# Kernel tuning notes

Measured on AMD Instinct MI355X. Metric: run time of the kernel, lower is better.

The kernel has to match this reference:

```python
import jax, jax.numpy as jnp
import numpy as np

B, L, D = 4, 2048, 1024
E, K, H = 8, 2, 4096
EPS = 1e-5


def setup_inputs() -> dict:
    key = jax.random.key(0)
    ks = jax.random.split(key, 6)
    x = jax.random.normal(ks[0], (B, L, D), jnp.float32)
    gate_w = jax.random.normal(ks[1], (E, D), jnp.float32) * 0.02
    W1 = jax.random.normal(ks[2], (E, D, H), jnp.float32) * 0.02
    b1 = jnp.zeros((E, H), jnp.float32)
    W2 = jax.random.normal(ks[3], (E, H, D), jnp.float32) * 0.02
    b2 = jnp.zeros((E, D), jnp.float32)
    gamma = jnp.ones((D,), jnp.float32)
    beta = jnp.zeros((D,), jnp.float32)
    return {"x": x, "gamma": gamma, "beta": beta, "gate_w": gate_w,
            "W1": W1, "b1": b1, "W2": W2, "b2": b2}


def reference(x, gamma, beta, gate_w, W1, b1, W2, b2):
    # LayerNorm (biased variance, eps=1e-5, matches torch.nn.LayerNorm)
    mu = jnp.mean(x, axis=-1, keepdims=True)
    var = jnp.mean((x - mu) ** 2, axis=-1, keepdims=True)
    xn = (x - mu) / jnp.sqrt(var + EPS) * gamma + beta
    xf = xn.reshape(-1, D)  # (T, D), T = B*L
    T = xf.shape[0]

    # gating: top-k logits -> softmax -> scatter into dense gates (T, E)
    logits = xf @ gate_w.T  # (T, E)
    top_v, top_i = jax.lax.top_k(logits, K)
    top_g = jax.nn.softmax(top_v, axis=-1)
    gates = jnp.zeros_like(logits).at[jnp.arange(T)[:, None], top_i].set(top_g)

    # experts: dense-equivalent of masked gather/FFN/scatter-add combine.
    # Non-selected experts contribute with gate weight 0 -> identical math.
    h = jax.nn.gelu(jnp.einsum('td,edh->teh', xf, W1) + b1, approximate=False)
    y = jnp.einsum('teh,ehd->ted', h, W2) + b2  # (T, E, D)
    out = jnp.einsum('te,ted->td', gates, y).reshape(B, L, D) + x

    # load-balance loss: MSE(mean gate per expert, uniform)
    load = jnp.mean(gates, axis=0)
    bal_loss = jnp.mean((load - 1.0 / E) ** 2)
    return out, bal_loss
```

## Files before the change

kernel.cpp:

```cpp
#include <hip/hip_runtime.h>
#include <hip/hip_bf16.h>

#define T_TOK 8192
#define DD 1024
#define EE 8
#define HH 4096
#define NA (2 * T_TOK)
#define NBLK (NA / 256)

typedef __bf16 bf16_t;
typedef __bf16 bf16x8 __attribute__((ext_vector_type(8)));
typedef __bf16 bf16x4 __attribute__((ext_vector_type(4)));
typedef float f32x4 __attribute__((ext_vector_type(4)));

#define GLDS(g, l) __builtin_amdgcn_global_load_lds( \
    (const __attribute__((address_space(1))) void*)(g), \
    (__attribute__((address_space(3))) void*)(l), 16, 0, 0)

__global__ __launch_bounds__(256) void ln_gate_kernel(
    const float* __restrict__ x, const float* __restrict__ gamma,
    const float* __restrict__ beta, const float* __restrict__ gate_w,
    bf16_t* __restrict__ xn, int* __restrict__ tokexp, float* __restrict__ tokgate)
{
    const int t = blockIdx.x;
    const int tid = threadIdx.x;
    const int lane = tid & 63, wave = tid >> 6;
    __shared__ float wred[4];
    __shared__ float stats[2];
    __shared__ float lred[32];
    __shared__ float logitsS[8];

    float4 v = ((const float4*)(x + (size_t)t * DD))[tid];
    float s = v.x + v.y + v.z + v.w;
#pragma unroll
    for (int o = 32; o > 0; o >>= 1) s += __shfl_down(s, o, 64);
    if (lane == 0) wred[wave] = s;
    __syncthreads();
    if (tid == 0) stats[0] = (wred[0] + wred[1] + wred[2] + wred[3]) * (1.0f / DD);
    __syncthreads();
    const float mu = stats[0];
    float d0 = v.x - mu, d1 = v.y - mu, d2 = v.z - mu, d3 = v.w - mu;
    float q = d0*d0 + d1*d1 + d2*d2 + d3*d3;
#pragma unroll
    for (int o = 32; o > 0; o >>= 1) q += __shfl_down(q, o, 64);
    __syncthreads();
    if (lane == 0) wred[wave] = q;
    __syncthreads();
    if (tid == 0) stats[1] = rsqrtf((wred[0]+wred[1]+wred[2]+wred[3]) * (1.0f / DD) + 1e-5f);
    __syncthreads();
    const float rstd = stats[1];
    float4 g4 = ((const float4*)gamma)[tid];
    float4 b4 = ((const float4*)beta)[tid];
    float n0 = d0 * rstd * g4.x + b4.x;
    float n1 = d1 * rstd * g4.y + b4.y;
    float n2 = d2 * rstd * g4.z + b4.z;
    float n3 = d3 * rstd * g4.w + b4.w;
    bf16x4 pk = { (bf16_t)n0, (bf16_t)n1, (bf16_t)n2, (bf16_t)n3 };
    ((bf16x4*)(xn + (size_t)t * DD))[tid] = pk;

    float part[8];
#pragma unroll
    for (int e = 0; e < 8; ++e) {
        float4 gw = ((const float4*)(gate_w + (size_t)e * DD))[tid];
        part[e] = n0 * gw.x + n1 * gw.y + n2 * gw.z + n3 * gw.w;
    }
#pragma unroll
    for (int e = 0; e < 8; ++e) {
        float p = part[e];
#pragma unroll
        for (int o = 32; o > 0; o >>= 1) p += __shfl_down(p, o, 64);
        if (lane == 0) lred[wave * 8 + e] = p;
    }
    __syncthreads();
    if (tid < 8) logitsS[tid] = lred[tid] + lred[8 + tid] + lred[16 + tid] + lred[24 + tid];
    __syncthreads();
    if (tid == 0) {
        float best = -1e30f; int e0 = 0;
        for (int e = 0; e < 8; ++e) { float le = logitsS[e]; if (le > best) { best = le; e0 = e; } }
        float best2 = -1e30f; int e1 = (e0 == 0) ? 1 : 0;
        for (int e = 0; e < 8; ++e) if (e != e0) { float le = logitsS[e]; if (le > best2) { best2 = le; e1 = e; } }
        float z = expf(best2 - best);
        float g0 = 1.0f / (1.0f + z);
        float g1 = z * g0;
        tokexp[2*t] = e0; tokexp[2*t+1] = e1;
        tokgate[2*t] = g0; tokgate[2*t+1] = g1;
    }
}

__global__ __launch_bounds__(256) void hist_kernel(
    const int* __restrict__ tokexp, const float* __restrict__ tokgate,
    int* __restrict__ blockcnt, float* __restrict__ blockgsum)
{
    __shared__ int hcnt[EE];
    __shared__ float hg[EE];
    const int b = blockIdx.x, tid = threadIdx.x;
    if (tid < EE) { hcnt[tid] = 0; hg[tid] = 0.f; }
    __syncthreads();
    int idx = b * 256 + tid;
    int e = tokexp[idx];
    atomicAdd(&hcnt[e], 1);
    atomicAdd(&hg[e], tokgate[idx]);
    __syncthreads();
    if (tid < EE) {
        blockcnt[b * EE + tid] = hcnt[tid];
        blockgsum[b * EE + tid] = hg[tid];
    }
}

__global__ __launch_bounds__(64) void offs_bal_kernel(
    const int* __restrict__ blockcnt, const float* __restrict__ blockgsum,
    int* __restrict__ cnt, int* __restrict__ offs, int* __restrict__ basep,
    float* __restrict__ bal_out)
{
    __shared__ int cntS[EE];
    const int tid = threadIdx.x;
    if (tid < EE) {
        int run = 0;
        for (int b = 0; b < NBLK; ++b) {
            basep[b * EE + tid] = run;
            run += blockcnt[b * EE + tid];
        }
        cnt[tid] = run;
        cntS[tid] = run;
    }
    __syncthreads();
    __shared__ int offsS[EE];
    if (tid == 0) {
        int run = 0; 
        for (int e = 0; e < EE; ++e) { offsS[e] = run; offs[e] = run; run += cntS[e]; }
        float bal = 0.f;
        for (int e = 0; e < EE; ++e) {
            float g = 0.f;
            for (int b = 0; b < NBLK; ++b) g += blockgsum[b * EE + e];
            float l = g * (1.0f / T_TOK) - (1.0f / EE);
            bal += l * l;
        }
        bal_out[0] = bal * (1.0f / EE);
    }
    __syncthreads();
    if (tid < EE) {
        for (int b = 0; b < NBLK; ++b) basep[b * EE + tid] += offsS[tid];
    }
}

__global__ __launch_bounds__(256) void scatter_kernel(
    const int* __restrict__ tokexp, const float* __restrict__ tokgate,
    const int* __restrict__ basep,
    int* __restrict__ tok, float* __restrict__ gatev, int* __restrict__ a_of_t)
{
    __shared__ int hcnt[EE];
    const int b = blockIdx.x, tid = threadIdx.x;
    if (tid < EE) hcnt[tid] = 0;
    __syncthreads();
    int idx = b * 256 + tid;
    int e = tokexp[idx];
    int r = atomicAdd(&hcnt[e], 1);
    int a = basep[b * EE + e] + r;
    tok[a] = idx >> 1;
    gatev[a] = tokgate[idx];
    a_of_t[idx] = a;
}

__global__ __launch_bounds__(256) void convT_kernel(
    const float* __restrict__ in, bf16_t* __restrict__ out, int R, int C)
{
    __shared__ float tile[64][65];
    int e = blockIdx.z;
    int c0 = blockIdx.x * 64, r0 = blockIdx.y * 64;
    int tx = threadIdx.x & 63, ty = threadIdx.x >> 6;
    const float* src = in + ((size_t)e * R + r0) * C + c0;
#pragma unroll
    for (int i = 0; i < 16; ++i) {
        int r = ty + i * 4;
        tile[r][tx] = src[(size_t)r * C + tx];
    }
    __syncthreads();
    bf16_t* dst = out + ((size_t)e * C + c0) * R + r0;
#pragma unroll
    for (int i = 0; i < 16; ++i) {
        int cc = ty + i * 4;
        dst[(size_t)cc * R + tx] = (bf16_t)tile[tx][cc];
    }
}

__global__ __launch_bounds__(256) void ffn1_kernel(
    const bf16_t* __restrict__ xn, const bf16_t* __restrict__ w1t,
    const float* __restrict__ b1, const int* __restrict__ tok,
    const int* __restrict__ cnt, const int* __restrict__ offs,
    bf16_t* __restrict__ h1)
{
    const int e = blockIdx.z;
    const int c = cnt[e];
    const int m0 = blockIdx.y * 128;
    if (m0 >= c) return;
    const int n0 = blockIdx.x * 128;
    const int off = offs[e];

    __shared__ __align__(16) bf16_t As[128 * 32];
    __shared__ __align__(16) bf16_t Bs[128 * 32];

    const int tid = threadIdx.x;
    const int sr = tid >> 2;
    const int scol = (tid & 3) * 8;

    int ar0 = m0 + sr;      if (ar0 >= c) ar0 = c - 1;
    int ar1 = m0 + 64 + sr; if (ar1 >= c) ar1 = c - 1;
    const bf16_t* aptr0 = xn + (size_t)tok[off + ar0] * DD + scol;
    const bf16_t* aptr1 = xn + (size_t)tok[off + ar1] * DD + scol;
    const bf16_t* bptr0 = w1t + ((size_t)e * HH + n0 + sr) * DD + scol;
    const bf16_t* bptr1 = bptr0 + (size_t)64 * DD;

    bf16_t* ldsA0 = As + (size_t)tid * 8;
    bf16_t* ldsA1 = As + (size_t)(256 + tid) * 8;
    bf16_t* ldsB0 = Bs + (size_t)tid * 8;
    bf16_t* ldsB1 = Bs + (size_t)(256 + tid) * 8;

    const int lane = tid & 63;
    const int wave = tid >> 6;
    const int wr = wave >> 1, wc = wave & 1;
    const int mL = lane & 15, quad = lane >> 4;

    const bf16_t* Abase = As + ((wr * 64 + mL) * 32 + quad * 8);
    const bf16_t* Bbase = Bs + ((wc * 64 + mL) * 32 + quad * 8);

    f32x4 acc[4][4] = {};

    for (int k0 = 0; k0 < DD; k0 += 32) {
        GLDS(aptr0, ldsA0);
        GLDS(aptr1, ldsA1);
        GLDS(bptr0, ldsB0);
        GLDS(bptr1, ldsB1);
        aptr0 += 32; aptr1 += 32; bptr0 += 32; bptr1 += 32;
        __syncthreads();
        bf16x8 af[4], bfv[4];
#pragma unroll
        for (int i = 0; i < 4; ++i) af[i] = *(const bf16x8*)(Abase + i * 16 * 32);
#pragma unroll
        for (int j = 0; j < 4; ++j) bfv[j] = *(const bf16x8*)(Bbase + j * 16 * 32);
#pragma unroll
        for (int i = 0; i < 4; ++i)
#pragma unroll
            for (int j = 0; j < 4; ++j)
                acc[i][j] = __builtin_amdgcn_mfma_f32_16x16x32_bf16(af[i], bfv[j], acc[i][j], 0, 0, 0);
        __syncthreads();
    }

    const float* b1e = b1 + (size_t)e * HH;
#pragma unroll
    for (int i = 0; i < 4; ++i) {
#pragma unroll
        for (int r = 0; r < 4; ++r) {
            int m = m0 + wr * 64 + i * 16 + quad * 4 + r;
            if (m < c) {
                bf16_t* hrow = h1 + (size_t)(off + m) * HH;
#pragma unroll
                for (int j = 0; j < 4; ++j) {
                    int n = n0 + wc * 64 + j * 16 + mL;
                    float v = acc[i][j][r] + b1e[n];
                    v = 0.5f * v * (1.0f + erff(v * 0.70710678118654752f));
                    hrow[n] = (bf16_t)v;
                }
            }
        }
    }
}

__global__ __launch_bounds__(256) void ffn2_kernel(
    const bf16_t* __restrict__ h1, const bf16_t* __restrict__ w2t,
    const float* __restrict__ b2, const float* __restrict__ gatev,
    const int* __restrict__ cnt, const int* __restrict__ offs,
    bf16_t* __restrict__ yv)
{
    const int e = blockIdx.z;
    const int c = cnt[e];
    const int m0 = blockIdx.y * 128;
    if (m0 >= c) return;
    const int n0 = blockIdx.x * 128;
    const int off = offs[e];

    __shared__ __align__(16) bf16_t As[128 * 32];
    __shared__ __align__(16) bf16_t Bs[128 * 32];

    const int tid = threadIdx.x;
    const int sr = tid >> 2;
    const int scol = (tid & 3) * 8;

    int ar0 = m0 + sr;      if (ar0 >= c) ar0 = c - 1;
    int ar1 = m0 + 64 + sr; if (ar1 >= c) ar1 = c - 1;
    const bf16_t* aptr0 = h1 + (size_t)(off + ar0) * HH + scol;
    const bf16_t* aptr1 = h1 + (size_t)(off + ar1) * HH + scol;
    const bf16_t* bptr0 = w2t + ((size_t)e * DD + n0 + sr) * HH + scol;
    const bf16_t* bptr1 = bptr0 + (size_t)64 * HH;

    bf16_t* ldsA0 = As + (size_t)tid * 8;
    bf16_t* ldsA1 = As + (size_t)(256 + tid) * 8;
    bf16_t* ldsB0 = Bs + (size_t)tid * 8;
    bf16_t* ldsB1 = Bs + (size_t)(256 + tid) * 8;

    const int lane = tid & 63;
    const int wave = tid >> 6;
    const int wr = wave >> 1, wc = wave & 1;
    const int mL = lane & 15, quad = lane >> 4;

    const bf16_t* Abase = As + ((wr * 64 + mL) * 32 + quad * 8);
    const bf16_t* Bbase = Bs + ((wc * 64 + mL) * 32 + quad * 8);

    f32x4 acc[4][4] = {};

    for (int k0 = 0; k0 < HH; k0 += 32) {
        GLDS(aptr0, ldsA0);
        GLDS(aptr1, ldsA1);
        GLDS(bptr0, ldsB0);
        GLDS(bptr1, ldsB1);
        aptr0 += 32; aptr1 += 32; bptr0 += 32; bptr1 += 32;
        __syncthreads();
        bf16x8 af[4], bfv[4];
#pragma unroll
        for (int i = 0; i < 4; ++i) af[i] = *(const bf16x8*)(Abase + i * 16 * 32);
#pragma unroll
        for (int j = 0; j < 4; ++j) bfv[j] = *(const bf16x8*)(Bbase + j * 16 * 32);
#pragma unroll
        for (int i = 0; i < 4; ++i)
#pragma unroll
            for (int j = 0; j < 4; ++j)
                acc[i][j] = __builtin_amdgcn_mfma_f32_16x16x32_bf16(af[i], bfv[j], acc[i][j], 0, 0, 0);
        __syncthreads();
    }

    const float* b2e = b2 + (size_t)e * DD;
#pragma unroll
    for (int i = 0; i < 4; ++i) {
#pragma unroll
        for (int r = 0; r < 4; ++r) {
            int m = m0 + wr * 64 + i * 16 + quad * 4 + r;
            if (m < c) {
                float g = gatev[off + m];
                bf16_t* yrow = yv + (size_t)(off + m) * DD;
#pragma unroll
                for (int j = 0; j < 4; ++j) {
                    int n = n0 + wc * 64 + j * 16 + mL;
                    float v = (acc[i][j][r] + b2e[n]) * g;
                    yrow[n] = (bf16_t)v;
                }
            }
        }
    }
}

__global__ __launch_bounds__(256) void combine_kernel(
    const float* __restrict__ x, const bf16_t* __restrict__ yv,
    const int* __restrict__ a_of_t, float* __restrict__ outp)
{
    int t = blockIdx.x;
    int tid = threadIdx.x;
    int a0 = a_of_t[2*t], a1 = a_of_t[2*t+1];
    float4 xv = ((const float4*)(x + (size_t)t * DD))[tid];
    bf16x4 y0 = ((const bf16x4*)(yv + (size_t)a0 * DD))[tid];
    bf16x4 y1 = ((const bf16x4*)(yv + (size_t)a1 * DD))[tid];
    float4 o;
    o.x = xv.x + (float)y0[0] + (float)y1[0];
    o.y = xv.y + (float)y0[1] + (float)y1[1];
    o.z = xv.z + (float)y0[2] + (float)y1[2];
    o.w = xv.w + (float)y0[3] + (float)y1[3];
    ((float4*)(outp + (size_t)t * DD))[tid] = o;
}

extern "C" void kernel_launch(void* const* d_in, const int* in_sizes, int n_in,
                              void* d_out, int out_size, void* d_ws, size_t ws_size,
                              hipStream_t stream)
{
    const float* x      = (const float*)d_in[0];
    const float* gamma  = (const float*)d_in[1];
    const float* beta   = (const float*)d_in[2];
    const float* gate_w = (const float*)d_in[3];
    const float* W1     = (const float*)d_in[4];
    const float* b1     = (const float*)d_in[5];
    const float* W2     = (const float*)d_in[6];
    const float* b2     = (const float*)d_in[7];
    float* outp = (float*)d_out;
    float* bal_out = outp + (size_t)T_TOK * DD;

    char* ws = (char*)d_ws;
    size_t off = 0;
    auto alloc = [&](size_t bytes) {
        char* p = ws + off;
        off += (bytes + 255) & ~(size_t)255;
        return p;
    };
    bf16_t* xn   = (bf16_t*)alloc((size_t)T_TOK * DD * 2);
    bf16_t* w1t  = (bf16_t*)alloc((size_t)EE * HH * DD * 2);
    bf16_t* w2t  = (bf16_t*)alloc((size_t)EE * DD * HH * 2);
    bf16_t* h1   = (bf16_t*)alloc((size_t)NA * HH * 2);
    bf16_t* yv   = (bf16_t*)alloc((size_t)NA * DD * 2);
    int*   tok     = (int*)alloc(NA * 4);
    float* gatev   = (float*)alloc(NA * 4);
    int*   a_of_t  = (int*)alloc(NA * 4);
    int*   tokexp  = (int*)alloc(NA * 4);
    float* tokgate = (float*)alloc(NA * 4);
    int*   blockcnt  = (int*)alloc(NBLK * EE * 4);
    float* blockgsum = (float*)alloc(NBLK * EE * 4);
    int*   basep     = (int*)alloc(NBLK * EE * 4);
    int*   cnt  = (int*)alloc(EE * 4);
    int*   offs = (int*)alloc(EE * 4);

    convT_kernel<<<dim3(HH/64, DD/64, EE), 256, 0, stream>>>(W1, w1t, DD, HH);
    convT_kernel<<<dim3(DD/64, HH/64, EE), 256, 0, stream>>>(W2, w2t, HH, DD);
    ln_gate_kernel<<<T_TOK, 256, 0, stream>>>(x, gamma, beta, gate_w, xn, tokexp, tokgate);
    hist_kernel<<<NBLK, 256, 0, stream>>>(tokexp, tokgate, blockcnt, blockgsum);
    offs_bal_kernel<<<1, 64, 0, stream>>>(blockcnt, blockgsum, cnt, offs, basep, bal_out);
    scatter_kernel<<<NBLK, 256, 0, stream>>>(tokexp, tokgate, basep, tok, gatev, a_of_t);
    ffn1_kernel<<<dim3(HH/128, 64, EE), 256, 0, stream>>>(xn, w1t, b1, tok, cnt, offs, h1);
    ffn2_kernel<<<dim3(DD/128, 64, EE), 256, 0, stream>>>(h1, w2t, b2, gatev, cnt, offs, yv);
    combine_kernel<<<T_TOK, 256, 0, stream>>>(x, yv, a_of_t, outp);
}
```

Measured before the change: 872.4 us.

## Enlarge MoE GEMM tiles to 256x256 with double-buffered swizzled LDS and fast GELU

Both expert GEMM kernels move from 128x128 tiles with K=32 to 256x256 tiles with K=64 and 512 threads. LDS is double-buffered so the global_load_lds for the next K slice overlaps MFMA work on the current one, and an XOR swizzle is applied to the LDS layout to avoid bank conflicts. The epilogue is vectorised, and the erf-based GELU is replaced by a tanh approximation built on exp2/rcp. Costs: 128KB of LDS per block, more padded work for experts whose token count is not a multiple of 256, and a GELU that no longer matches the exact erf form.

```diff
diff --git a/kernel.cpp b/kernel.cpp
--- a/kernel.cpp
+++ b/kernel.cpp
@@ -16,6 +16,14 @@
 #define GLDS(g, l) __builtin_amdgcn_global_load_lds( \
     (const __attribute__((address_space(1))) void*)(g), \
     (__attribute__((address_space(3))) void*)(l), 16, 0, 0)
+
+__device__ __forceinline__ float gelu_fast(float v) {
+    float u = v * (0.79788456080286536f + 0.035677408136300125f * v * v);
+    float a = 2.8853900817779268f * u;
+    a = fminf(fmaxf(a, -87.0f), 87.0f);
+    float t = __builtin_amdgcn_exp2f(a);
+    return v * t * __builtin_amdgcn_rcpf(t + 1.0f);
+}
 
 __global__ __launch_bounds__(256) void ln_gate_kernel(
     const float* __restrict__ x, const float* __restrict__ gamma,
@@ -183,7 +191,8 @@
     }
 }
 
-__global__ __launch_bounds__(256) void ffn1_kernel(
+
+__global__ __launch_bounds__(512, 2) void ffn1_kernel(
     const bf16_t* __restrict__ xn, const bf16_t* __restrict__ w1t,
     const float* __restrict__ b1, const int* __restrict__ tok,
     const int* __restrict__ cnt, const int* __restrict__ offs,
@@ -191,81 +200,110 @@
 {
     const int e = blockIdx.z;
     const int c = cnt[e];
-    const int m0 = blockIdx.y * 128;
+    const int m0 = blockIdx.y * 256;
     if (m0 >= c) return;
-    const int n0 = blockIdx.x * 128;
+    const int n0 = blockIdx.x * 256;
     const int off = offs[e];
 
-    __shared__ __align__(16) bf16_t As[128 * 32];
-    __shared__ __align__(16) bf16_t Bs[128 * 32];
+    __shared__ __align__(16) bf16_t As[2][256 * 64];
+    __shared__ __align__(16) bf16_t Bs[2][256 * 64];
 
     const int tid = threadIdx.x;
-    const int sr = tid >> 2;
-    const int scol = (tid & 3) * 8;
-
-    int ar0 = m0 + sr;      if (ar0 >= c) ar0 = c - 1;
-    int ar1 = m0 + 64 + sr; if (ar1 >= c) ar1 = c - 1;
-    const bf16_t* aptr0 = xn + (size_t)tok[off + ar0] * DD + scol;
-    const bf16_t* aptr1 = xn + (size_t)tok[off + ar1] * DD + scol;
-    const bf16_t* bptr0 = w1t + ((size_t)e * HH + n0 + sr) * DD + scol;
-    const bf16_t* bptr1 = bptr0 + (size_t)64 * DD;
-
-    bf16_t* ldsA0 = As + (size_t)tid * 8;
-    bf16_t* ldsA1 = As + (size_t)(256 + tid) * 8;
-    bf16_t* ldsB0 = Bs + (size_t)tid * 8;
-    bf16_t* ldsB1 = Bs + (size_t)(256 + tid) * 8;
-
-    const int lane = tid & 63;
-    const int wave = tid >> 6;
-    const int wr = wave >> 1, wc = wave & 1;
-    const int mL = lane & 15, quad = lane >> 4;
-
-    const bf16_t* Abase = As + ((wr * 64 + mL) * 32 + quad * 8);
-    const bf16_t* Bbase = Bs + ((wc * 64 + mL) * 32 + quad * 8);
-
-    f32x4 acc[4][4] = {};
-
-    for (int k0 = 0; k0 < DD; k0 += 32) {
-        GLDS(aptr0, ldsA0);
-        GLDS(aptr1, ldsA1);
-        GLDS(bptr0, ldsB0);
-        GLDS(bptr1, ldsB1);
-        aptr0 += 32; aptr1 += 32; bptr0 += 32; bptr1 += 32;
-        __syncthreads();
-        bf16x8 af[4], bfv[4];
-#pragma unroll
-        for (int i = 0; i < 4; ++i) af[i] = *(const bf16x8*)(Abase + i * 16 * 32);
-#pragma unroll
-        for (int j = 0; j < 4; ++j) bfv[j] = *(const bf16x8*)(Bbase + j * 16 * 32);
-#pragma unroll
-        for (int i = 0; i < 4; ++i)
-#pragma unroll
-            for (int j = 0; j < 4; ++j)
-                acc[i][j] = __builtin_amdgcn_mfma_f32_16x16x32_bf16(af[i], bfv[j], acc[i][j], 0, 0, 0);
-        __syncthreads();
+    const int rloc = tid >> 3;
+    const int qx8 = ((tid & 7) ^ (rloc & 7)) * 8;
+
+    int mA0 = m0 + rloc;        if (mA0 >= c) mA0 = c - 1;
+    int mA1 = m0 + 64 + rloc;   if (mA1 >= c) mA1 = c - 1;
+    int mA2 = m0 + 128 + rloc;  if (mA2 >= c) mA2 = c - 1;
+    int mA3 = m0 + 192 + rloc;  if (mA3 >= c) mA3 = c - 1;
+    const bf16_t* pa0 = xn + (size_t)tok[off + mA0] * DD + qx8;
+    const bf16_t* pa1 = xn + (size_t)tok[off + mA1] * DD + qx8;
+    const bf16_t* pa2 = xn + (size_t)tok[off + mA2] * DD + qx8;
+    const bf16_t* pa3 = xn + (size_t)tok[off + mA3] * DD + qx8;
+    const bf16_t* pb0 = w1t + ((size_t)e * HH + n0 + rloc) * DD + qx8;
+    const bf16_t* pb1 = pb0 + (size_t)64 * DD;
+    const bf16_t* pb2 = pb0 + (size_t)128 * DD;
+    const bf16_t* pb3 = pb0 + (size_t)192 * DD;
+
+    const int lane = tid & 63, wave = tid >> 6;
+    const int wm = wave >> 2, wn = wave & 3;
+    const int l15 = lane & 15, lq = lane >> 4;
+    const int rx = l15 & 7;
+    const int rowA = (wm * 128 + l15) * 64;
+    const int rowB = (wn * 64 + l15) * 64;
+    const int cs0 = ((0 + lq) ^ rx) * 8;
+    const int cs1 = ((4 + lq) ^ rx) * 8;
+
+    f32x4 acc[8][4] = {};
+
+    auto stage = [&](int buf) {
+        bf16_t* la = &As[buf][tid * 8];
+        bf16_t* lb = &Bs[buf][tid * 8];
+        GLDS(pa0, la);          GLDS(pa1, la + 4096);
+        GLDS(pa2, la + 8192);   GLDS(pa3, la + 12288);
+        GLDS(pb0, lb);          GLDS(pb1, lb + 4096);
+        GLDS(pb2, lb + 8192);   GLDS(pb3, lb + 12288);
+        pa0 += 64; pa1 += 64; pa2 += 64; pa3 += 64;
+        pb0 += 64; pb1 += 64; pb2 += 64; pb3 += 64;
+    };
+
+    stage(0);
+    const int NT = DD / 64;
+    for (int t = 0; t < NT; ++t) {
+        const int cur = t & 1;
+        if (t + 1 < NT) {
+            stage(cur ^ 1);
+            asm volatile("s_waitcnt vmcnt(8)" ::: "memory");
+        } else {
+            asm volatile("s_waitcnt vmcnt(0)" ::: "memory");
+        }
+        __builtin_amdgcn_s_barrier();
+        const bf16_t* Ab = &As[cur][0];
+        const bf16_t* Bb = &Bs[cur][0];
+#pragma unroll
+        for (int kk = 0; kk < 2; ++kk) {
+            const int cs = kk ? cs1 : cs0;
+            bf16x8 wf[4], xf[8];
+#pragma unroll
+            for (int nf = 0; nf < 4; ++nf)
+                wf[nf] = *(const bf16x8*)(Bb + rowB + nf * 1024 + cs);
+#pragma unroll
+            for (int tf = 0; tf < 8; ++tf)
+                xf[tf] = *(const bf16x8*)(Ab + rowA + tf * 1024 + cs);
+#pragma unroll
+            for (int tf = 0; tf < 8; ++tf)
+#pragma unroll
+                for (int nf = 0; nf < 4; ++nf)
+                    acc[tf][nf] = __builtin_amdgcn_mfma_f32_16x16x32_bf16(
+                        wf[nf], xf[tf], acc[tf][nf], 0, 0, 0);
+        }
+        asm volatile("s_waitcnt lgkmcnt(0)" ::: "memory");
+        __builtin_amdgcn_s_barrier();
     }
 
     const float* b1e = b1 + (size_t)e * HH;
 #pragma unroll
-    for (int i = 0; i < 4; ++i) {
-#pragma unroll
-        for (int r = 0; r < 4; ++r) {
-            int m = m0 + wr * 64 + i * 16 + quad * 4 + r;
-            if (m < c) {
-                bf16_t* hrow = h1 + (size_t)(off + m) * HH;
-#pragma unroll
-                for (int j = 0; j < 4; ++j) {
-                    int n = n0 + wc * 64 + j * 16 + mL;
-                    float v = acc[i][j][r] + b1e[n];
-                    v = 0.5f * v * (1.0f + erff(v * 0.70710678118654752f));
-                    hrow[n] = (bf16_t)v;
-                }
+    for (int tf = 0; tf < 8; ++tf) {
+        int m = m0 + wm * 128 + tf * 16 + l15;
+        if (m < c) {
+            bf16_t* hrow = h1 + (size_t)(off + m) * HH;
+#pragma unroll
+            for (int nf = 0; nf < 4; ++nf) {
+                int n = n0 + wn * 64 + nf * 16 + lq * 4;
+                float4 bb = *(const float4*)(b1e + n);
+                f32x4 a = acc[tf][nf];
+                bf16x4 pk;
+                pk[0] = (bf16_t)gelu_fast(a[0] + bb.x);
+                pk[1] = (bf16_t)gelu_fast(a[1] + bb.y);
+                pk[2] = (bf16_t)gelu_fast(a[2] + bb.z);
+                pk[3] = (bf16_t)gelu_fast(a[3] + bb.w);
+                *(bf16x4*)(hrow + n) = pk;
             }
         }
     }
 }
 
-__global__ __launch_bounds__(256) void ffn2_kernel(
+__global__ __launch_bounds__(512, 2) void ffn2_kernel(
     const bf16_t* __restrict__ h1, const bf16_t* __restrict__ w2t,
     const float* __restrict__ b2, const float* __restrict__ gatev,
     const int* __restrict__ cnt, const int* __restrict__ offs,
@@ -273,75 +311,105 @@
 {
     const int e = blockIdx.z;
     const int c = cnt[e];
-    const int m0 = blockIdx.y * 128;
+    const int m0 = blockIdx.y * 256;
     if (m0 >= c) return;
-    const int n0 = blockIdx.x * 128;
+    const int n0 = blockIdx.x * 256;
     const int off = offs[e];
 
-    __shared__ __align__(16) bf16_t As[128 * 32];
-    __shared__ __align__(16) bf16_t Bs[128 * 32];
+    __shared__ __align__(16) bf16_t As[2][256 * 64];
+    __shared__ __align__(16) bf16_t Bs[2][256 * 64];
 
     const int tid = threadIdx.x;
-    const int sr = tid >> 2;
-    const int scol = (tid & 3) * 8;
-
-    int ar0 = m0 + sr;      if (ar0 >= c) ar0 = c - 1;
-    int ar1 = m0 + 64 + sr; if (ar1 >= c) ar1 = c - 1;
-    const bf16_t* aptr0 = h1 + (size_t)(off + ar0) * HH + scol;
-    const bf16_t* aptr1 = h1 + (size_t)(off + ar1) * HH + scol;
-    const bf16_t* bptr0 = w2t + ((size_t)e * DD + n0 + sr) * HH + scol;
-    const bf16_t* bptr1 = bptr0 + (size_t)64 * HH;
-
-    bf16_t* ldsA0 = As + (size_t)tid * 8;
-    bf16_t* ldsA1 = As + (size_t)(256 + tid) * 8;
-    bf16_t* ldsB0 = Bs + (size_t)tid * 8;
-    bf16_t* ldsB1 = Bs + (size_t)(256 + tid) * 8;
-
-    const int lane = tid & 63;
-    const int wave = tid >> 6;
-    const int wr = wave >> 1, wc = wave & 1;
-    const int mL = lane & 15, quad = lane >> 4;
-
-    const bf16_t* Abase = As + ((wr * 64 + mL) * 32 + quad * 8);
-    const bf16_t* Bbase = Bs + ((wc * 64 + mL) * 32 + quad * 8);
-
-    f32x4 acc[4][4] = {};
-
-    for (int k0 = 0; k0 < HH; k0 += 32) {
-        GLDS(aptr0, ldsA0);
-        GLDS(aptr1, ldsA1);
-        GLDS(bptr0, ldsB0);
-        GLDS(bptr1, ldsB1);
-        aptr0 += 32; aptr1 += 32; bptr0 += 32; bptr1 += 32;
-        __syncthreads();
-        bf16x8 af[4], bfv[4];
-#pragma unroll
-        for (int i = 0; i < 4; ++i) af[i] = *(const bf16x8*)(Abase + i * 16 * 32);
-#pragma unroll
-        for (int j = 0; j < 4; ++j) bfv[j] = *(const bf16x8*)(Bbase + j * 16 * 32);
-#pragma unroll
-        for (int i = 0; i < 4; ++i)
-#pragma unroll
-            for (int j = 0; j < 4; ++j)
-                acc[i][j] = __builtin_amdgcn_mfma_f32_16x16x32_bf16(af[i], bfv[j], acc[i][j], 0, 0, 0);
-        __syncthreads();
+    const int rloc = tid >> 3;
+    const int qx8 = ((tid & 7) ^ (rloc & 7)) * 8;
+
+    int mA0 = m0 + rloc;        if (mA0 >= c) mA0 = c - 1;
+    int mA1 = m0 + 64 + rloc;   if (mA1 >= c) mA1 = c - 1;
+    int mA2 = m0 + 128 + rloc;  if (mA2 >= c) mA2 = c - 1;
+    int mA3 = m0 + 192 + rloc;  if (mA3 >= c) mA3 = c - 1;
+    const bf16_t* pa0 = h1 + (size_t)(off + mA0) * HH + qx8;
+    const bf16_t* pa1 = h1 + (size_t)(off + mA1) * HH + qx8;
+    const bf16_t* pa2 = h1 + (size_t)(off + mA2) * HH + qx8;
+    const bf16_t* pa3 = h1 + (size_t)(off + mA3) * HH + qx8;
+    const bf16_t* pb0 = w2t + ((size_t)e * DD + n0 + rloc) * HH + qx8;
+    const bf16_t* pb1 = pb0 + (size_t)64 * HH;
+    const bf16_t* pb2 = pb0 + (size_t)128 * HH;
+    const bf16_t* pb3 = pb0 + (size_t)192 * HH;
+
+    const int lane = tid & 63, wave = tid >> 6;
+    const int wm = wave >> 2, wn = wave & 3;
+    const int l15 = lane & 15, lq = lane >> 4;
+    const int rx = l15 & 7;
+    const int rowA = (wm * 128 + l15) * 64;
+    const int rowB = (wn * 64 + l15) * 64;
+    const int cs0 = ((0 + lq) ^ rx) * 8;
+    const int cs1 = ((4 + lq) ^ rx) * 8;
+
+    f32x4 acc[8][4] = {};
+
+    auto stage = [&](int buf) {
+        bf16_t* la = &As[buf][tid * 8];
+        bf16_t* lb = &Bs[buf][tid * 8];
+        GLDS(pa0, la);          GLDS(pa1, la + 4096);
+        GLDS(pa2, la + 8192);   GLDS(pa3, la + 12288);
+        GLDS(pb0, lb);          GLDS(pb1, lb + 4096);
+        GLDS(pb2, lb + 8192);   GLDS(pb3, lb + 12288);
+        pa0 += 64; pa1 += 64; pa2 += 64; pa3 += 64;
+        pb0 += 64; pb1 += 64; pb2 += 64; pb3 += 64;
+    };
+
+    stage(0);
+    const int NT = HH / 64;
+    for (int t = 0; t < NT; ++t) {
+        const int cur = t & 1;
+        if (t + 1 < NT) {
+            stage(cur ^ 1);
+            asm volatile("s_waitcnt vmcnt(8)" ::: "memory");
+        } else {
+            asm volatile("s_waitcnt vmcnt(0)" ::: "memory");
+        }
+        __builtin_amdgcn_s_barrier();
+        const bf16_t* Ab = &As[cur][0];
+        const bf16_t* Bb = &Bs[cur][0];
+#pragma unroll
+        for (int kk = 0; kk < 2; ++kk) {
+            const int cs = kk ? cs1 : cs0;
+            bf16x8 wf[4], xf[8];
+#pragma unroll
+            for (int nf = 0; nf < 4; ++nf)
+                wf[nf] = *(const bf16x8*)(Bb + rowB + nf * 1024 + cs);
+#pragma unroll
+            for (int tf = 0; tf < 8; ++tf)
+                xf[tf] = *(const bf16x8*)(Ab + rowA + tf * 1024 + cs);
+#pragma unroll
+            for (int tf = 0; tf < 8; ++tf)
+#pragma unroll
+                for (int nf = 0; nf < 4; ++nf)
+                    acc[tf][nf] = __builtin_amdgcn_mfma_f32_16x16x32_bf16(
+                        wf[nf], xf[tf], acc[tf][nf], 0, 0, 0);
+        }
+        asm volatile("s_waitcnt lgkmcnt(0)" ::: "memory");
+        __builtin_amdgcn_s_barrier();
     }
 
     const float* b2e = b2 + (size_t)e * DD;
 #pragma unroll
-    for (int i = 0; i < 4; ++i) {
-#pragma unroll
-        for (int r = 0; r < 4; ++r) {
-            int m = m0 + wr * 64 + i * 16 + quad * 4 + r;
-            if (m < c) {
-                float g = gatev[off + m];
-                bf16_t* yrow = yv + (size_t)(off + m) * DD;
-#pragma unroll
-                for (int j = 0; j < 4; ++j) {
-                    int n = n0 + wc * 64 + j * 16 + mL;
-                    float v = (acc[i][j][r] + b2e[n]) * g;
-                    yrow[n] = (bf16_t)v;
-                }
+    for (int tf = 0; tf < 8; ++tf) {
+        int m = m0 + wm * 128 + tf * 16 + l15;
+        if (m < c) {
+            float g = gatev[off + m];
+            bf16_t* yrow = yv + (size_t)(off + m) * DD;
+#pragma unroll
+            for (int nf = 0; nf < 4; ++nf) {
+                int n = n0 + wn * 64 + nf * 16 + lq * 4;
+                float4 bb = *(const float4*)(b2e + n);
+                f32x4 a = acc[tf][nf];
+                bf16x4 pk;
+                pk[0] = (bf16_t)((a[0] + bb.x) * g);
+                pk[1] = (bf16_t)((a[1] + bb.y) * g);
+                pk[2] = (bf16_t)((a[2] + bb.z) * g);
+                pk[3] = (bf16_t)((a[3] + bb.w) * g);
+                *(bf16x4*)(yrow + n) = pk;
             }
         }
     }
@@ -409,7 +477,7 @@
     hist_kernel<<<NBLK, 256, 0, stream>>>(tokexp, tokgate, blockcnt, blockgsum);
     offs_bal_kernel<<<1, 64, 0, stream>>>(blockcnt, blockgsum, cnt, offs, basep, bal_out);
     scatter_kernel<<<NBLK, 256, 0, stream>>>(tokexp, tokgate, basep, tok, gatev, a_of_t);
-    ffn1_kernel<<<dim3(HH/128, 64, EE), 256, 0, stream>>>(xn, w1t, b1, tok, cnt, offs, h1);
-    ffn2_kernel<<<dim3(DD/128, 64, EE), 256, 0, stream>>>(h1, w2t, b2, gatev, cnt, offs, yv);
+    ffn1_kernel<<<dim3(HH/256, 32, EE), 512, 0, stream>>>(xn, w1t, b1, tok, cnt, offs, h1);
+    ffn2_kernel<<<dim3(DD/256, 32, EE), 512, 0, stream>>>(h1, w2t, b2, gatev, cnt, offs, yv);
     combine_kernel<<<T_TOK, 256, 0, stream>>>(x, yv, a_of_t, outp);
 }
```

Measured after the change: 868.5 us. About the same (-0.4%).
